# Optimization experiments

Measured on AMD Instinct MI355X. Metric: run time of the kernel, lower is better.

Reference implementation:

```python
import jax, jax.numpy as jnp
import numpy as np

B, T, HID = 1, 2048, 1024
H, D, S, KMAX = 16, 64, 64, 8


def local_attention(q, k, v, W):
    # lucidrains LocalAttention: causal, look_backward=1, autopad, scale=D**-0.5
    b, h, t, d = q.shape
    pad = (-t) % W
    qp = jnp.pad(q, ((0, 0), (0, 0), (0, pad), (0, 0)))
    kp = jnp.pad(k, ((0, 0), (0, 0), (0, pad), (0, 0)))
    vp = jnp.pad(v, ((0, 0), (0, 0), (0, pad), (0, 0)))
    tp = t + pad
    nw = tp // W
    qw = qp.reshape(b, h, nw, W, d)
    kw = kp.reshape(b, h, nw, W, d)
    vw = vp.reshape(b, h, nw, W, d)

    def look_back(x):  # prepend previous window (zeros for window 0)
        prev = jnp.pad(x, ((0, 0), (0, 0), (1, 0), (0, 0), (0, 0)))[:, :, :nw]
        return jnp.concatenate([prev, x], axis=3)  # (b,h,nw,2W,d)

    kk, vv = look_back(kw), look_back(vw)
    pos = jnp.arange(tp).reshape(nw, W)
    kpos = jnp.concatenate(
        [jnp.pad(pos, ((1, 0), (0, 0)), constant_values=-1)[:nw], pos], axis=1)  # (nw,2W)
    scores = jnp.einsum('bhnwd,bhnkd->bhnwk', qw, kk) * (d ** -0.5)
    valid = (pos[:, :, None] >= kpos[:, None, :]) & (kpos[:, None, :] >= 0)
    scores = jnp.where(valid[None, None], scores, -jnp.finfo(scores.dtype).max)
    probs = jax.nn.softmax(scores, axis=-1)
    out = jnp.einsum('bhnwk,bhnkd->bhnwd', probs, vv).reshape(b, h, tp, d)
    return out[:, :, :t]


def setup_inputs() -> dict:
    key = jax.random.key(0)
    ks = jax.random.split(key, 9)
    sd = 0.02
    return {
        'hidden_states': jax.random.normal(ks[0], (B, T, HID), jnp.float32),
        'Wq': jax.random.normal(ks[1], (HID, H * D), jnp.float32) * sd,
        'Wk': jax.random.normal(ks[2], (HID, H * D), jnp.float32) * sd,
        'Wv': jax.random.normal(ks[3], (HID, H * D), jnp.float32) * sd,
        'Wo': jax.random.normal(ks[4], (H * D, HID), jnp.float32) * sd,
        'Wc': jax.random.normal(ks[5], (S * D, D), jnp.float32) * sd,
        'bc': jax.random.normal(ks[6], (D,), jnp.float32) * sd,
        'k_scale': jnp.ones((1, H, 1), jnp.float32),
        'k_bias': jnp.zeros((1, H, 1), jnp.float32),
        'Wg': jax.random.normal(ks[7], (HID, 3 * H), jnp.float32) * sd,
        'bg': jax.random.normal(ks[8], (3 * H,), jnp.float32) * sd,
    }


def reference(hidden_states, Wq, Wk, Wv, Wo, Wc, bc, k_scale, k_bias, Wg, bg):
    b, t, _ = hidden_states.shape
    scale = D ** -0.5
    q = (hidden_states @ Wq).reshape(b, t, H, D).transpose(0, 2, 1, 3)
    k = (hidden_states @ Wk).reshape(b, t, H, D).transpose(0, 2, 1, 3)
    v = (hidden_states @ Wv).reshape(b, t, H, D).transpose(0, 2, 1, 3)

    sw_out = local_attention(q, k, v, S)

    pad = (-t) % S
    qp = jnp.pad(q, ((0, 0), (0, 0), (0, pad), (0, 0)))
    kp = jnp.pad(k, ((0, 0), (0, 0), (0, pad), (0, 0)))
    vp = jnp.pad(v, ((0, 0), (0, 0), (0, pad), (0, 0)))
    tp = t + pad
    nb = tp // S

    # compressed branch: shared compress MLP for k and v (same weights in torch)
    k_blk = kp.reshape(b, H, nb, S * D)
    v_blk = vp.reshape(b, H, nb, S * D)
    kc = jax.nn.gelu(k_blk @ Wc + bc, approximate=False)  # (b,H,nb,D)
    vc = jax.nn.gelu(v_blk @ Wc + bc, approximate=False)

    importance = jnp.einsum('bhid,bhjd->bhij', qp, kc) * scale  # (b,H,tp,nb)
    comp_probs = jax.nn.softmax(importance, axis=-1)
    comp_out = jnp.einsum('bhij,bhjd->bhid', comp_probs, vc)[:, :, :t]

    # block scores, entropy-driven dynamic top-k
    block_scores = importance.reshape(b, H, nb, S, nb).mean(axis=3)  # (b,H,nb,nb)
    block_probs = jax.nn.softmax(block_scores, axis=-1)
    entropy = -jnp.sum(block_probs * jnp.log(block_probs + 1e-9), axis=-1)
    max_entropy = jnp.log(jnp.float32(nb))
    norm_entropy = entropy / (max_entropy + 1e-9)  # (b,H,nb)
    k_logit = k_scale * norm_entropy + k_bias
    k_ratio = jax.nn.sigmoid(k_logit)
    dynamic_k = jnp.clip(KMAX * k_ratio, 1, KMAX).astype(jnp.int32)
    avg_k = dynamic_k.astype(jnp.float32).mean()

    _, topk_idx = jax.lax.top_k(block_scores, KMAX)  # (b,H,nb,KMAX)
    k_mask = jnp.arange(KMAX)[None, None, None, :] < dynamic_k[..., None]
    sel = (topk_idx[..., None] == jnp.arange(nb)) & k_mask[..., None]  # (b,H,nb,K,nb)
    mask = sel.any(axis=-2) | jnp.eye(nb, dtype=bool)  # (b,H,nb,nb)
    sparse_mask = jnp.repeat(jnp.repeat(mask, S, axis=2), S, axis=3)  # (b,H,tp,tp)

    attn = jnp.einsum('bhid,bhjd->bhij', qp, kp) * scale
    attn = jnp.where(sparse_mask, attn, -jnp.finfo(attn.dtype).max)
    fine_probs = jax.nn.softmax(attn, axis=-1)
    fine_out = jnp.einsum('bhij,bhjd->bhid', fine_probs, vp)[:, :, :t]

    gate = jax.nn.sigmoid(hidden_states @ Wg + bg)  # (b,t,3H)
    gate = gate.reshape(b, t, H, 3).transpose(0, 2, 1, 3)  # (b,H,t,3)
    combined = jnp.stack([sw_out, comp_out, fine_out], axis=-1)  # (b,H,t,D,3)
    out = jnp.einsum('bhnds,bhns->bhnd', combined, gate)
    merged = out.transpose(0, 2, 1, 3).reshape(b, t, H * D)
    output = merged @ Wo
    return output, avg_k, k_ratio, norm_entropy
```

## Files before the change

### kernel.cpp

```cpp
#include <hip/hip_runtime.h>
#include <math.h>

#define TT 2048
#define NH 16
#define HD 64
#define NB 32
#define HIDDEN 1024

typedef short s8v __attribute__((ext_vector_type(8)));
typedef float f4v __attribute__((ext_vector_type(4)));

__device__ __forceinline__ unsigned short f2bf(float x){
  unsigned u = __float_as_uint(x);
  unsigned r = (u + 0x7fffu + ((u>>16)&1u)) >> 16;
  return (unsigned short)r;
}
__device__ __forceinline__ float bf2f(unsigned short b){
  return __uint_as_float(((unsigned)b)<<16);
}
__device__ __forceinline__ void bsplit(float x, unsigned short& h, unsigned short& l){
  h = f2bf(x);
  l = f2bf(x - bf2f(h));
}

__device__ __forceinline__ float rmax32(float v){
#pragma unroll
  for(int o=16;o>0;o>>=1) v = fmaxf(v, __shfl_xor(v,o,32));
  return v;
}
__device__ __forceinline__ float rsum32(float v){
#pragma unroll
  for(int o=16;o>0;o>>=1) v += __shfl_xor(v,o,32);
  return v;
}

__global__ __launch_bounds__(256) void split_hs_k(
    const float* __restrict__ hs, unsigned short* __restrict__ hh, unsigned short* __restrict__ hl)
{
  int i = (blockIdx.x*256 + threadIdx.x)*4;
  float4 x = *(const float4*)(hs + i);
  ushort4 hv, lv;
  bsplit(x.x, hv.x, lv.x); bsplit(x.y, hv.y, lv.y);
  bsplit(x.z, hv.z, lv.z); bsplit(x.w, hv.w, lv.w);
  *(ushort4*)(hh + i) = hv;
  *(ushort4*)(hl + i) = lv;
}

__global__ __launch_bounds__(256) void prep_w_k(
    const float* __restrict__ Wq, const float* __restrict__ Wk,
    const float* __restrict__ Wv, const float* __restrict__ Wo,
    unsigned short* __restrict__ wth, unsigned short* __restrict__ wtl,
    unsigned short* __restrict__ woth)
{
  int z = blockIdx.z;
  const float* W = (z==0)?Wq:((z==1)?Wk:((z==2)?Wv:Wo));
  int k0 = blockIdx.y*64, n0 = blockIdx.x*64;
  __shared__ float L[64][68];
  int t = threadIdx.x;
  int rr = t>>2, cg = t&3;
  const float* src = W + (size_t)(k0+rr)*1024 + n0 + cg*16;
  float4 a = *(const float4*)(src);
  float4 b = *(const float4*)(src+4);
  float4 c = *(const float4*)(src+8);
  float4 d = *(const float4*)(src+12);
  *(float4*)&L[rr][cg*16+0]  = a;
  *(float4*)&L[rr][cg*16+4]  = b;
  *(float4*)&L[rr][cg*16+8]  = c;
  *(float4*)&L[rr][cg*16+12] = d;
  __syncthreads();
  int nr = t>>2, kg = t&3;
  unsigned short hb[16], lb[16];
#pragma unroll
  for(int j=0;j<16;j++){
    float v = L[kg*16+j][nr];
    bsplit(v, hb[j], lb[j]);
  }
  if(z<3){
    size_t orow = ((size_t)z*1024 + n0 + nr)*1024 + k0 + kg*16;
    *(ushort4*)(wth+orow+0)  = make_ushort4(hb[0],hb[1],hb[2],hb[3]);
    *(ushort4*)(wth+orow+4)  = make_ushort4(hb[4],hb[5],hb[6],hb[7]);
    *(ushort4*)(wth+orow+8)  = make_ushort4(hb[8],hb[9],hb[10],hb[11]);
    *(ushort4*)(wth+orow+12) = make_ushort4(hb[12],hb[13],hb[14],hb[15]);
    *(ushort4*)(wtl+orow+0)  = make_ushort4(lb[0],lb[1],lb[2],lb[3]);
    *(ushort4*)(wtl+orow+4)  = make_ushort4(lb[4],lb[5],lb[6],lb[7]);
    *(ushort4*)(wtl+orow+8)  = make_ushort4(lb[8],lb[9],lb[10],lb[11]);
    *(ushort4*)(wtl+orow+12) = make_ushort4(lb[12],lb[13],lb[14],lb[15]);
  }else{
    size_t orow = ((size_t)n0 + nr)*1024 + k0 + kg*16;
    *(ushort4*)(woth+orow+0)  = make_ushort4(hb[0],hb[1],hb[2],hb[3]);
    *(ushort4*)(woth+orow+4)  = make_ushort4(hb[4],hb[5],hb[6],hb[7]);
    *(ushort4*)(woth+orow+8)  = make_ushort4(hb[8],hb[9],hb[10],hb[11]);
    *(ushort4*)(woth+orow+12) = make_ushort4(hb[12],hb[13],hb[14],hb[15]);
  }
}

__global__ __launch_bounds__(256) void prep_wc_k(
    const float* __restrict__ Wc, unsigned short* __restrict__ wcth, unsigned short* __restrict__ wctl)
{
  int k0 = blockIdx.x*64;
  __shared__ float L[64][68];
  int t = threadIdx.x;
  int rr = t>>2, cg = t&3;
  const float* src = Wc + (size_t)(k0+rr)*64 + cg*16;
  float4 a = *(const float4*)(src);
  float4 b = *(const float4*)(src+4);
  float4 c = *(const float4*)(src+8);
  float4 d = *(const float4*)(src+12);
  *(float4*)&L[rr][cg*16+0]  = a;
  *(float4*)&L[rr][cg*16+4]  = b;
  *(float4*)&L[rr][cg*16+8]  = c;
  *(float4*)&L[rr][cg*16+12] = d;
  __syncthreads();
  int nr = t>>2, kg = t&3;
  unsigned short hb[16], lb[16];
#pragma unroll
  for(int j=0;j<16;j++){
    float v = L[kg*16+j][nr];
    bsplit(v, hb[j], lb[j]);
  }
  size_t orow = (size_t)nr*4096 + k0 + kg*16;
  *(ushort4*)(wcth+orow+0)  = make_ushort4(hb[0],hb[1],hb[2],hb[3]);
  *(ushort4*)(wcth+orow+4)  = make_ushort4(hb[4],hb[5],hb[6],hb[7]);
  *(ushort4*)(wcth+orow+8)  = make_ushort4(hb[8],hb[9],hb[10],hb[11]);
  *(ushort4*)(wcth+orow+12) = make_ushort4(hb[12],hb[13],hb[14],hb[15]);
  *(ushort4*)(wctl+orow+0)  = make_ushort4(lb[0],lb[1],lb[2],lb[3]);
  *(ushort4*)(wctl+orow+4)  = make_ushort4(lb[4],lb[5],lb[6],lb[7]);
  *(ushort4*)(wctl+orow+8)  = make_ushort4(lb[8],lb[9],lb[10],lb[11]);
  *(ushort4*)(wctl+orow+12) = make_ushort4(lb[12],lb[13],lb[14],lb[15]);
}

#define LROW 40
__global__ __launch_bounds__(256) void mfma_qkv_k(
    const unsigned short* __restrict__ ahg, const unsigned short* __restrict__ alg,
    const unsigned short* __restrict__ bhg, const unsigned short* __restrict__ blg,
    float* __restrict__ C0, float* __restrict__ C1, float* __restrict__ C2)
{
  __shared__ unsigned short Ah[128*LROW], Al[128*LROW], Bh[128*LROW], Bl[128*LROW];
  int tid = threadIdx.x;
  int bn = blockIdx.x*128, bm = blockIdx.y*128;
  bool tp = (blockIdx.x < 16);
  int sr = tid>>2, skg = tid&3;
  const unsigned short* gA  = ahg + (size_t)(bm+sr)*HIDDEN + skg*8;
  const unsigned short* gAl = alg + (size_t)(bm+sr)*HIDDEN + skg*8;
  const unsigned short* gB  = bhg + (size_t)(bn+sr)*HIDDEN + skg*8;
  const unsigned short* gBl = blg + (size_t)(bn+sr)*HIDDEN + skg*8;
  int wv = tid>>6, ln = tid&63;
  int wm = (wv&1)*64, wn = (wv>>1)*64;
  int fr = ln&15, fq = ln>>4;
  int wlds = sr*LROW + skg*8;
  f4v acc[4][4] = {};
  for(int k0=0;k0<HIDDEN;k0+=32){
    s8v a0 = *(const s8v*)(gA + k0);
    s8v a1 = *(const s8v*)(gA + 65536 + k0);
    s8v b0 = *(const s8v*)(gB + k0);
    s8v b1 = *(const s8v*)(gB + 65536 + k0);
    s8v a0l, a1l, b0l, b1l;
    if(tp){
      a0l = *(const s8v*)(gAl + k0);
      a1l = *(const s8v*)(gAl + 65536 + k0);
      b0l = *(const s8v*)(gBl + k0);
      b1l = *(const s8v*)(gBl + 65536 + k0);
    }
    __syncthreads();
    *(s8v*)&Ah[wlds] = a0; *(s8v*)&Ah[wlds + 64*LROW] = a1;
    *(s8v*)&Bh[wlds] = b0; *(s8v*)&Bh[wlds + 64*LROW] = b1;
    if(tp){
      *(s8v*)&Al[wlds] = a0l; *(s8v*)&Al[wlds + 64*LROW] = a1l;
      *(s8v*)&Bl[wlds] = b0l; *(s8v*)&Bl[wlds + 64*LROW] = b1l;
    }
    __syncthreads();
    s8v af[4], bf[4], tf;
#pragma unroll
    for(int i=0;i<4;i++) af[i] = *(const s8v*)&Ah[(wm+i*16+fr)*LROW + fq*8];
#pragma unroll
    for(int i=0;i<4;i++) bf[i] = *(const s8v*)&Bh[(wn+i*16+fr)*LROW + fq*8];
#pragma unroll
    for(int i=0;i<4;i++)
#pragma unroll
      for(int j=0;j<4;j++)
        acc[i][j] = __builtin_amdgcn_mfma_f32_16x16x32_bf16(af[i], bf[j], acc[i][j], 0,0,0);
    if(tp){
#pragma unroll
      for(int i=0;i<4;i++){
        tf = *(const s8v*)&Al[(wm+i*16+fr)*LROW + fq*8];
#pragma unroll
        for(int j=0;j<4;j++)
          acc[i][j] = __builtin_amdgcn_mfma_f32_16x16x32_bf16(tf, bf[j], acc[i][j], 0,0,0);
      }
#pragma unroll
      for(int j=0;j<4;j++){
        tf = *(const s8v*)&Bl[(wn+j*16+fr)*LROW + fq*8];
#pragma unroll
        for(int i=0;i<4;i++)
          acc[i][j] = __builtin_amdgcn_mfma_f32_16x16x32_bf16(af[i], tf, acc[i][j], 0,0,0);
      }
    }
  }
  int z = bn >> 10;
  float* C = (z==0)?C0:((z==1)?C1:C2);
#pragma unroll
  for(int i=0;i<4;i++){
    int mb = bm + wm + i*16 + fq*4;
#pragma unroll
    for(int j=0;j<4;j++){
      int n = bn + wn + j*16 + fr;
      int n1 = n & 1023, hd = n1>>6, d = n1&63;
      float* dst = C + ((size_t)hd*TT + mb)*HD + d;
#pragma unroll
      for(int r=0;r<4;r++) dst[(size_t)r*HD] = acc[i][j][r];
    }
  }
}

__global__ __launch_bounds__(256) void conv_qkv(
    const float* __restrict__ qb, const float* __restrict__ kb, const float* __restrict__ vb,
    unsigned short* __restrict__ qbh, unsigned short* __restrict__ qbl,
    unsigned short* __restrict__ kbh, unsigned short* __restrict__ kbl,
    unsigned short* __restrict__ vbh)
{
  int z = blockIdx.y;
  const float* s = (z==0)?qb:((z==1)?kb:vb);
  unsigned short* dh = (z==0)?qbh:((z==1)?kbh:vbh);
  unsigned short* dl = (z==0)?qbl:kbl;
  size_t i = ((size_t)blockIdx.x*256 + threadIdx.x)*8;
  float4 a = *(const float4*)(s+i);
  float4 b = *(const float4*)(s+i+4);
  float xs[8] = {a.x,a.y,a.z,a.w,b.x,b.y,b.z,b.w};
  s8v rh, rl;
#pragma unroll
  for(int u=0;u<8;u++){
    unsigned short h = f2bf(xs[u]);
    rh[u] = (short)h;
    rl[u] = (short)f2bf(xs[u] - bf2f(h));
  }
  *(s8v*)(dh+i) = rh;
  if(z<2) *(s8v*)(dl+i) = rl;
}

__global__ __launch_bounds__(256) void conv_vt(
    const float* __restrict__ vb, unsigned short* __restrict__ vth)
{
  int tt = blockIdx.x, h = blockIdx.y;
  __shared__ float L[64][68];
  int t = threadIdx.x;
  int row = t>>2, dg = (t&3)*16;
  const float* src = vb + ((size_t)h*TT + tt*64 + row)*HD + dg;
  float4 a = *(const float4*)(src);
  float4 b = *(const float4*)(src+4);
  float4 c = *(const float4*)(src+8);
  float4 e = *(const float4*)(src+12);
  *(float4*)&L[row][dg+0]  = a;
  *(float4*)&L[row][dg+4]  = b;
  *(float4*)&L[row][dg+8]  = c;
  *(float4*)&L[row][dg+12] = e;
  __syncthreads();
  int d = t>>2, kg = (t&3)*16;
  s8v r0, r1;
#pragma unroll
  for(int u=0;u<8;u++)  r0[u] = (short)f2bf(L[kg+u][d]);
#pragma unroll
  for(int u=0;u<8;u++)  r1[u] = (short)f2bf(L[kg+8+u][d]);
  unsigned short* dst = vth + ((size_t)h*HD + d)*TT + tt*64 + kg;
  *(s8v*)(dst)   = r0;
  *(s8v*)(dst+8) = r1;
}

#define CROW 40
__global__ __launch_bounds__(256) void mfma_compress_k(
    const unsigned short* __restrict__ kbh, const unsigned short* __restrict__ kbl,
    const unsigned short* __restrict__ vbh,
    const unsigned short* __restrict__ wcth, const unsigned short* __restrict__ wctl,
    float* __restrict__ ccpart)
{
  __shared__ unsigned short As[64*CROW], Al[64*CROW], Bs[64*CROW], Bl[64*CROW];
  int chunk = blockIdx.x;
  int mt = blockIdx.y;
  bool isK = (mt < 8);
  const unsigned short* Ag  = isK ? (kbh + (size_t)mt*262144) : (vbh + (size_t)(mt-8)*262144);
  const unsigned short* Agl = kbl + (size_t)(isK ? mt : 0)*262144;
  int tid = threadIdx.x;
  int sr = tid>>2, skg = (tid&3)*8;
  int k0b = chunk*512;
  const unsigned short* gA  = Ag  + (size_t)sr*4096 + k0b + skg;
  const unsigned short* gAl = Agl + (size_t)sr*4096 + k0b + skg;
  const unsigned short* gB  = wcth + (size_t)sr*4096 + k0b + skg;
  const unsigned short* gBl = wctl + (size_t)sr*4096 + k0b + skg;
  int wv = tid>>6, ln = tid&63;
  int fr = ln&15, fq = ln>>4;
  int wlds = sr*CROW + skg;
  f4v acc[4] = {};
  for(int ks=0; ks<512; ks+=32){
    s8v a0 = *(const s8v*)(gA + ks);
    s8v b0 = *(const s8v*)(gB + ks);
    s8v b1 = *(const s8v*)(gBl + ks);
    s8v a1 = {};
    if(isK) a1 = *(const s8v*)(gAl + ks);
    __syncthreads();
    *(s8v*)&As[wlds] = a0;
    *(s8v*)&Bs[wlds] = b0;
    *(s8v*)&Bl[wlds] = b1;
    if(isK) *(s8v*)&Al[wlds] = a1;
    __syncthreads();
    s8v bfh = *(const s8v*)&Bs[(wv*16+fr)*CROW + fq*8];
    s8v bfl = *(const s8v*)&Bl[(wv*16+fr)*CROW + fq*8];
#pragma unroll
    for(int m=0;m<4;m++){
      s8v af = *(const s8v*)&As[(m*16+fr)*CROW + fq*8];
      acc[m] = __builtin_amdgcn_mfma_f32_16x16x32_bf16(af, bfh, acc[m], 0,0,0);
      acc[m] = __builtin_amdgcn_mfma_f32_16x16x32_bf16(af, bfl, acc[m], 0,0,0);
      if(isK){
        s8v afl = *(const s8v*)&Al[(m*16+fr)*CROW + fq*8];
        acc[m] = __builtin_amdgcn_mfma_f32_16x16x32_bf16(afl, bfh, acc[m], 0,0,0);
      }
    }
  }
  float* dst = ccpart + ((size_t)chunk*1024 + mt*64)*64;
#pragma unroll
  for(int m=0;m<4;m++)
#pragma unroll
    for(int r=0;r<4;r++)
      dst[(size_t)(m*16+fq*4+r)*64 + wv*16 + fr] = acc[m][r];
}

__global__ __launch_bounds__(256) void compress_fin(
    const float* __restrict__ ccpart, const float* __restrict__ bcp,
    unsigned short* __restrict__ kch, unsigned short* __restrict__ kcl,
    unsigned short* __restrict__ vcth)
{
  int idx = blockIdx.x*256 + threadIdx.x;
  int row = idx>>6, col = idx&63;
  float s = 0.f;
#pragma unroll
  for(int c=0;c<8;c++) s += ccpart[(size_t)c*65536 + idx];
  s += bcp[col];
  float g = 0.5f*s*(1.f+erff(s*0.70710678118654752f));
  if(row < 512){
    unsigned short hi = f2bf(g);
    kch[idx] = hi;
    kcl[idx] = f2bf(g - bf2f(hi));
  }else{
    int r = row - 512;
    int h = r>>5, j = r&31;
    vcth[((size_t)h*64 + col)*32 + j] = f2bf(g);
  }
}

__global__ __launch_bounds__(256) void comp_attn_mfma(
    const unsigned short* __restrict__ qbh, const unsigned short* __restrict__ qbl,
    const unsigned short* __restrict__ kch, const unsigned short* __restrict__ kcl,
    const unsigned short* __restrict__ vcth,
    float* __restrict__ imp, float* __restrict__ comp)
{
  __shared__ unsigned short Pl[4*16*40];
  int tid = threadIdx.x;
  int wave = __builtin_amdgcn_readfirstlane(tid>>6);
  int ln = tid&63;
  int fr = ln&15, fq = ln>>4;
  int i = blockIdx.x, h = blockIdx.y;

  const unsigned short* qrh = qbh + ((size_t)h*TT + i*64 + wave*16 + fr)*HD + fq*8;
  const unsigned short* qrl = qbl + ((size_t)h*TT + i*64 + wave*16 + fr)*HD + fq*8;
  s8v bh0 = *(const s8v*)(qrh);
  s8v bh1 = *(const s8v*)(qrh + 32);
  s8v bl0 = *(const s8v*)(qrl);
  s8v bl1 = *(const s8v*)(qrl + 32);

  f4v sv[2] = {};
#pragma unroll
  for(int mt=0;mt<2;mt++){
    const unsigned short* ar = kch + ((size_t)h*32 + mt*16 + fr)*HD + fq*8;
    const unsigned short* al = kcl + ((size_t)h*32 + mt*16 + fr)*HD + fq*8;
    s8v ah0 = *(const s8v*)(ar);
    s8v ah1 = *(const s8v*)(ar + 32);
    s8v al0 = *(const s8v*)(al);
    s8v al1 = *(const s8v*)(al + 32);
    sv[mt] = __builtin_amdgcn_mfma_f32_16x16x32_bf16(ah0, bh0, sv[mt], 0,0,0);
    sv[mt] = __builtin_amdgcn_mfma_f32_16x16x32_bf16(ah1, bh1, sv[mt], 0,0,0);
    sv[mt] = __builtin_amdgcn_mfma_f32_16x16x32_bf16(al0, bh0, sv[mt], 0,0,0);
    sv[mt] = __builtin_amdgcn_mfma_f32_16x16x32_bf16(al1, bh1, sv[mt], 0,0,0);
    sv[mt] = __builtin_amdgcn_mfma_f32_16x16x32_bf16(ah0, bl0, sv[mt], 0,0,0);
    sv[mt] = __builtin_amdgcn_mfma_f32_16x16x32_bf16(ah1, bl1, sv[mt], 0,0,0);
  }
  int t = i*64 + wave*16 + fr;
  float* impr = imp + ((size_t)h*TT + t)*NB;
  float mx = -3.4e38f;
#pragma unroll
  for(int mt=0;mt<2;mt++)
#pragma unroll
    for(int r=0;r<4;r++){
      float s = sv[mt][r]*0.125f;
      sv[mt][r] = s;
      impr[mt*16 + fq*4 + r] = s;
      mx = fmaxf(mx, s);
    }
  mx = fmaxf(mx, __shfl_xor(mx,16,64));
  mx = fmaxf(mx, __shfl_xor(mx,32,64));
  unsigned short* Pw = Pl + wave*16*40;
  float es = 0.f;
#pragma unroll
  for(int mt=0;mt<2;mt++)
#pragma unroll
    for(int r=0;r<4;r++){
      float p = __expf(sv[mt][r] - mx);
      es += p;
      Pw[fr*40 + mt*16 + fq*4 + r] = f2bf(p);
    }
  es += __shfl_xor(es,16,64);
  es += __shfl_xor(es,32,64);

  s8v ap = *(const s8v*)&Pw[fr*40 + fq*8];
  f4v acc[4] = {};
#pragma unroll
  for(int nt=0;nt<4;nt++){
    s8v bv = *(const s8v*)(vcth + ((size_t)h*64 + nt*16 + fr)*32 + fq*8);
    acc[nt] = __builtin_amdgcn_mfma_f32_16x16x32_bf16(ap, bv, acc[nt], 0,0,0);
  }
  float lv[4];
#pragma unroll
  for(int r=0;r<4;r++) lv[r] = __shfl(es, fq*4+r, 64);
#pragma unroll
  for(int nt=0;nt<4;nt++)
#pragma unroll
    for(int r=0;r<4;r++){
      int tq = i*64 + wave*16 + fq*4 + r;
      comp[((size_t)h*TT + tq)*HD + nt*16 + fr] = acc[nt][r]/lv[r];
    }
}

__global__ __launch_bounds__(256) void mfma_proj_k(
    const unsigned short* __restrict__ ahg, const unsigned short* __restrict__ bhg,
    float* __restrict__ C)
{
  __shared__ unsigned short Ah[128*LROW], Bh[128*LROW];
  int tid = threadIdx.x;
  int bn = blockIdx.x*128, bm = blockIdx.y*128;
  int sr = tid>>2, skg = tid&3;
  const unsigned short* gA = ahg + (size_t)(bm+sr)*HIDDEN + skg*8;
  const unsigned short* gB = bhg + (size_t)(bn+sr)*HIDDEN + skg*8;
  int wv = tid>>6, ln = tid&63;
  int wm = (wv&1)*64, wn = (wv>>1)*64;
  int fr = ln&15, fq = ln>>4;
  int wlds = sr*LROW + skg*8;
  f4v acc[4][4] = {};
  for(int k0=0;k0<HIDDEN;k0+=32){
    s8v a0 = *(const s8v*)(gA + k0);
    s8v a1 = *(const s8v*)(gA + 65536 + k0);
    s8v b0 = *(const s8v*)(gB + k0);
    s8v b1 = *(const s8v*)(gB + 65536 + k0);
    __syncthreads();
    *(s8v*)&Ah[wlds] = a0; *(s8v*)&Ah[wlds + 64*LROW] = a1;
    *(s8v*)&Bh[wlds] = b0; *(s8v*)&Bh[wlds + 64*LROW] = b1;
    __syncthreads();
    s8v af[4], bf[4];
#pragma unroll
    for(int i=0;i<4;i++) af[i] = *(const s8v*)&Ah[(wm+i*16+fr)*LROW + fq*8];
#pragma unroll
    for(int i=0;i<4;i++) bf[i] = *(const s8v*)&Bh[(wn+i*16+fr)*LROW + fq*8];
#pragma unroll
    for(int i=0;i<4;i++)
#pragma unroll
      for(int j=0;j<4;j++)
        acc[i][j] = __builtin_amdgcn_mfma_f32_16x16x32_bf16(af[i], bf[j], acc[i][j], 0,0,0);
  }
#pragma unroll
  for(int i=0;i<4;i++){
    int mb = bm + wm + i*16 + fq*4;
#pragma unroll
    for(int j=0;j<4;j++){
      int n = bn + wn + j*16 + fr;
      float* dst = C + (size_t)mb*HIDDEN + n;
#pragma unroll
      for(int r=0;r<4;r++) dst[(size_t)r*HIDDEN] = acc[i][j][r];
    }
  }
}

__global__ __launch_bounds__(256) void gate_kernel(
    const float* __restrict__ hs, const float* __restrict__ Wg, const float* __restrict__ bg,
    float* __restrict__ gatep)
{
  int t = blockIdx.x;
  __shared__ float row[1024];
  __shared__ float red[4][64];
  int tid = threadIdx.x;
  *(float4*)(row + tid*4) = *(const float4*)(hs + (size_t)t*HIDDEN + tid*4);
  __syncthreads();
  int n = tid & 63, part = tid>>6;
  float s = 0.f;
  if(n < 48){
    const float* w = Wg + n;
    for(int kx = part*256; kx < part*256+256; kx++)
      s += row[kx]*w[(size_t)kx*48];
  }
  red[part][n] = s;
  __syncthreads();
  if(part==0 && n<48){
    float x = red[0][n]+red[1][n]+red[2][n]+red[3][n] + bg[n];
    gatep[(size_t)t*48 + n] = 1.f/(1.f+expf(-x));
  }
}

__global__ __launch_bounds__(256) void block_stats(
    const float* __restrict__ imp, const float* __restrict__ ksc, const float* __restrict__ kbi,
    unsigned* __restrict__ maskb, float* __restrict__ dkf,
    float* __restrict__ out_kratio, float* __restrict__ out_nent)
{
  int hb = blockIdx.x; int h = hb>>5, i = hb&31;
  int tid = threadIdx.x; int j = tid&31, p = tid>>5;
  const float* base = imp + ((size_t)h*TT + i*64)*NB;
  float s = 0.f;
  for(int t2=p*8; t2<p*8+8; t2++) s += base[(size_t)t2*NB + j];
  __shared__ float red[8][32];
  red[p][j] = s;
  __syncthreads();
  if(tid < 32){
    float bs = 0.f;
#pragma unroll
    for(int pp=0; pp<8; pp++) bs += red[pp][j];
    bs *= (1.f/64.f);
    float m = rmax32(bs);
    float e = expf(bs - m);
    float se = rsum32(e);
    float prob = e/se;
    float ent = rsum32(-prob * logf(prob + 1e-9f));
    float nent = ent / (3.4657359027997265f + 1e-9f);
    float kl = ksc[h]*nent + kbi[h];
    float kr = 1.f/(1.f + expf(-kl));
    float dkfl = fminf(fmaxf(8.f*kr, 1.f), 8.f);
    int dk = (int)dkfl;
    unsigned sel = 0u;
    for(int r=0;r<dk;r++){
      bool unpicked = ((sel>>j)&1u)==0u;
      float cand = unpicked ? bs : -3.4e38f;
      float mx = rmax32(cand);
      unsigned long long b = __ballot(cand == mx);
      int idxsel = __ffsll(b & 0xffffffffull) - 1;
      sel |= (1u<<idxsel);
    }
    sel |= (1u<<i);
    if(j==0){
      maskb[hb] = sel;
      dkf[hb] = (float)dk;
      out_kratio[hb] = kr;
      out_nent[hb] = nent;
    }
  }
}

__global__ __launch_bounds__(256) void avgk_kernel(const float* __restrict__ dkf, float* __restrict__ outp){
  __shared__ float red[256];
  int tid=threadIdx.x;
  red[tid] = dkf[tid] + dkf[tid+256];
  __syncthreads();
  for(int s=128;s>0;s>>=1){ if(tid<s) red[tid]+=red[tid+s]; __syncthreads(); }
  if(tid==0) outp[0] = red[0] * (1.f/512.f);
}

__global__ __launch_bounds__(256) void attn_mfma(
    const unsigned short* __restrict__ qbh, const unsigned short* __restrict__ kbh,
    const unsigned short* __restrict__ vth,
    const unsigned* __restrict__ maskb, float* __restrict__ outp, int causal_local)
{
  __shared__ unsigned short Kb[64*72];
  __shared__ unsigned short Vt[64*72];
  __shared__ unsigned short Pl[4*16*72];
  int tid = threadIdx.x;
  int wave = __builtin_amdgcn_readfirstlane(tid>>6);
  int ln = tid & 63;
  int fr = ln & 15, fq = ln >> 4;
  int hb = blockIdx.x; int h = hb>>5, i = hb&31;
  unsigned mb = causal_local ? ((1u<<i) | (i ? (1u<<(i-1)) : 0u)) : maskb[hb];

  const unsigned short* qrow = qbh + ((size_t)h*TT + i*64 + wave*16 + fr)*HD + fq*8;
  s8v bq0 = *(const s8v*)(qrow);
  s8v bq1 = *(const s8v*)(qrow + 32);

  f4v acc_o[4] = {};
  float m_run = -3.4e38f;
  float l_run = 0.f;

  int srow = tid>>2, sg = (tid&3)*16;
  unsigned short* Pw = Pl + wave*16*72;

  for(int j=0;j<NB;j++){
    if(!((mb>>j)&1u)) continue;
    __syncthreads();
    {
      const unsigned short* ks_ = kbh + ((size_t)h*TT + j*64 + srow)*HD + sg;
      *(s8v*)&Kb[srow*72 + sg]     = *(const s8v*)(ks_);
      *(s8v*)&Kb[srow*72 + sg + 8] = *(const s8v*)(ks_ + 8);
      const unsigned short* vs_ = vth + ((size_t)h*HD + srow)*TT + j*64 + sg;
      *(s8v*)&Vt[srow*72 + sg]     = *(const s8v*)(vs_);
      *(s8v*)&Vt[srow*72 + sg + 8] = *(const s8v*)(vs_ + 8);
    }
    __syncthreads();

    f4v sv[4] = {};
#pragma unroll
    for(int mt=0;mt<4;mt++){
      s8v ak0 = *(const s8v*)&Kb[(mt*16+fr)*72 + fq*8];
      s8v ak1 = *(const s8v*)&Kb[(mt*16+fr)*72 + fq*8 + 32];
      sv[mt] = __builtin_amdgcn_mfma_f32_16x16x32_bf16(ak0, bq0, sv[mt], 0,0,0);
      sv[mt] = __builtin_amdgcn_mfma_f32_16x16x32_bf16(ak1, bq1, sv[mt], 0,0,0);
    }
    bool diag = (causal_local!=0) && (j==i);
    int qpos = wave*16 + fr;
#pragma unroll
    for(int mt=0;mt<4;mt++){
#pragma unroll
      for(int r=0;r<4;r++){
        float s = sv[mt][r]*0.125f;
        if(diag && (mt*16 + fq*4 + r) > qpos) s = -3.4e38f;
        sv[mt][r] = s;
      }
    }
    float mx = -3.4e38f;
#pragma unroll
    for(int mt=0;mt<4;mt++)
#pragma unroll
      for(int r=0;r<4;r++) mx = fmaxf(mx, sv[mt][r]);
    mx = fmaxf(mx, __shfl_xor(mx,16,64));
    mx = fmaxf(mx, __shfl_xor(mx,32,64));
    float mnew = fmaxf(m_run, mx);
    float es = 0.f;
#pragma unroll
    for(int mt=0;mt<4;mt++)
#pragma unroll
      for(int r=0;r<4;r++){
        float p = __expf(sv[mt][r] - mnew);
        es += p;
        Pw[fr*72 + mt*16 + fq*4 + r] = f2bf(p);
      }
    es += __shfl_xor(es,16,64);
    es += __shfl_xor(es,32,64);
    float alpha = __expf(m_run - mnew);
    l_run = l_run*alpha + es;
    m_run = mnew;
    float av[4];
#pragma unroll
    for(int r=0;r<4;r++) av[r] = __shfl(alpha, fq*4+r, 64);
#pragma unroll
    for(int nt=0;nt<4;nt++)
#pragma unroll
      for(int r=0;r<4;r++) acc_o[nt][r] *= av[r];
    __syncthreads();

    s8v ap0 = *(const s8v*)&Pw[fr*72 + fq*8];
    s8v ap1 = *(const s8v*)&Pw[fr*72 + fq*8 + 32];
#pragma unroll
    for(int nt=0;nt<4;nt++){
      s8v bv0 = *(const s8v*)&Vt[(nt*16+fr)*72 + fq*8];
      s8v bv1 = *(const s8v*)&Vt[(nt*16+fr)*72 + fq*8 + 32];
      acc_o[nt] = __builtin_amdgcn_mfma_f32_16x16x32_bf16(ap0, bv0, acc_o[nt], 0,0,0);
      acc_o[nt] = __builtin_amdgcn_mfma_f32_16x16x32_bf16(ap1, bv1, acc_o[nt], 0,0,0);
    }
  }
  float lv[4];
#pragma unroll
  for(int r=0;r<4;r++) lv[r] = __shfl(l_run, fq*4+r, 64);
#pragma unroll
  for(int nt=0;nt<4;nt++){
#pragma unroll
    for(int r=0;r<4;r++){
      int t = i*64 + wave*16 + fq*4 + r;
      int d = nt*16 + fr;
      outp[((size_t)h*TT + t)*HD + d] = acc_o[nt][r] / lv[r];
    }
  }
}

__global__ __launch_bounds__(256) void combine_kernel(
    const float* __restrict__ swo, const float* __restrict__ comp, const float* __restrict__ fino,
    const float* __restrict__ gatep, unsigned short* __restrict__ mergedh)
{
  int idx = blockIdx.x*256 + threadIdx.x;
  int t = idx>>10, c = idx & 1023;
  int h = c>>6, d = c&63;
  const float* g = gatep + (size_t)t*48 + h*3;
  size_t a = ((size_t)h*TT + t)*HD + d;
  mergedh[idx] = f2bf(g[0]*swo[a] + g[1]*comp[a] + g[2]*fino[a]);
}

extern "C" void kernel_launch(void* const* d_in, const int* in_sizes, int n_in,
                              void* d_out, int out_size, void* d_ws, size_t ws_size,
                              hipStream_t stream) {
  (void)in_sizes; (void)n_in; (void)out_size; (void)ws_size;
  const float* hs  = (const float*)d_in[0];
  const float* Wq  = (const float*)d_in[1];
  const float* Wk  = (const float*)d_in[2];
  const float* Wv  = (const float*)d_in[3];
  const float* Wo  = (const float*)d_in[4];
  const float* Wc  = (const float*)d_in[5];
  const float* bcp = (const float*)d_in[6];
  const float* ksc = (const float*)d_in[7];
  const float* kbi = (const float*)d_in[8];
  const float* Wg  = (const float*)d_in[9];
  const float* bg  = (const float*)d_in[10];
  float* out = (float*)d_out;

  float* ws = (float*)d_ws;
  float* qb     = ws;
  float* kb     = qb + 2097152;
  float* vb     = kb + 2097152;
  float* gatep  = vb + 2097152;
  unsigned short* kch  = (unsigned short*)(gatep + 98304);
  unsigned short* kcl  = kch + 32768;
  unsigned short* vcth = kcl + 32768;
  float* imp    = gatep + 98304 + 65536;
  float* comp   = imp + 1048576;
  float* swo    = comp + 2097152;
  float* fino   = swo + 2097152;
  unsigned short* mergedh = (unsigned short*)(fino + 2097152);
  float* dkf    = fino + 2097152 + 1048576;
  unsigned* maskb = (unsigned*)(dkf + 512);
  unsigned short* woth = (unsigned short*)(dkf + 1024);
  unsigned short* qbh = (unsigned short*)(dkf + 1024 + 524288);
  unsigned short* kbh = qbh + 2097152;
  unsigned short* vth = kbh + 2097152;
  unsigned short* qbl = vth + 2097152;
  unsigned short* kbl = qbl + 2097152;
  unsigned short* vbh = kbl + 2097152;
  unsigned short* wcth = vbh + 2097152;
  unsigned short* wctl = wcth + 262144;
  float* ccpart = (float*)(wctl + 262144);

  unsigned short* hsh = (unsigned short*)comp;
  unsigned short* hsl = (unsigned short*)(comp + 1048576);
  unsigned short* wth = (unsigned short*)swo;
  unsigned short* wtl = (unsigned short*)(swo + 1572864);

  float* out_avgk   = out + 2097152;
  float* out_kratio = out + 2097153;
  float* out_nent   = out + 2097665;

  split_hs_k<<<dim3(2048), 256, 0, stream>>>(hs, hsh, hsl);
  prep_w_k<<<dim3(16,16,4), 256, 0, stream>>>(Wq, Wk, Wv, Wo, wth, wtl, woth);
  prep_wc_k<<<dim3(64), 256, 0, stream>>>(Wc, wcth, wctl);
  mfma_qkv_k<<<dim3(24,16), 256, 0, stream>>>(hsh, hsl, wth, wtl, qb, kb, vb);
  conv_qkv<<<dim3(1024,3), 256, 0, stream>>>(qb, kb, vb, qbh, qbl, kbh, kbl, vbh);
  conv_vt<<<dim3(32,16), 256, 0, stream>>>(vb, vth);
  gate_kernel<<<dim3(2048), 256, 0, stream>>>(hs, Wg, bg, gatep);
  mfma_compress_k<<<dim3(8,16), 256, 0, stream>>>(kbh, kbl, vbh, wcth, wctl, ccpart);
  compress_fin<<<dim3(256), 256, 0, stream>>>(ccpart, bcp, kch, kcl, vcth);
  comp_attn_mfma<<<dim3(32,16), 256, 0, stream>>>(qbh, qbl, kch, kcl, vcth, imp, comp);
  block_stats<<<dim3(512), 256, 0, stream>>>(imp, ksc, kbi, maskb, dkf, out_kratio, out_nent);
  avgk_kernel<<<dim3(1), 256, 0, stream>>>(dkf, out_avgk);
  attn_mfma<<<dim3(512), 256, 0, stream>>>(qbh, kbh, vth, maskb, swo, 1);
  attn_mfma<<<dim3(512), 256, 0, stream>>>(qbh, kbh, vth, maskb, fino, 0);
  combine_kernel<<<dim3(8192), 256, 0, stream>>>(swo, comp, fino, gatep, mergedh);
  mfma_proj_k<<<dim3(8,16), 256, 0, stream>>>(mergedh, woth, out);
}
```

Baseline: 259.3 us.

## Fuse prep kernels, QKV conversion epilogue, and sliding/fine attention with gating combine

Merges the three weight/activation prep kernels into one launch. The QKV GEMM epilogue now writes the bf16 hi/lo splits directly, which removes the fp32 QKV buffers and the conv_qkv pass, and conv_vt now reads bf16. The sliding-window and selected-block attention passes become one kernel that loads each K/V tile once for both softmax streams and applies the gate combine inline, so the swo/fino intermediates and combine_kernel are gone. The cost is more registers and LDS in the fused attention kernel, and uncoalesced 2-byte scattered stores in the GEMM epilogue.

```diff
diff --git a/kernel.cpp b/kernel.cpp
--- a/kernel.cpp
+++ b/kernel.cpp
@@ -34,106 +34,110 @@
   return v;
 }
 
-__global__ __launch_bounds__(256) void split_hs_k(
-    const float* __restrict__ hs, unsigned short* __restrict__ hh, unsigned short* __restrict__ hl)
-{
-  int i = (blockIdx.x*256 + threadIdx.x)*4;
-  float4 x = *(const float4*)(hs + i);
-  ushort4 hv, lv;
-  bsplit(x.x, hv.x, lv.x); bsplit(x.y, hv.y, lv.y);
-  bsplit(x.z, hv.z, lv.z); bsplit(x.w, hv.w, lv.w);
-  *(ushort4*)(hh + i) = hv;
-  *(ushort4*)(hl + i) = lv;
-}
-
-__global__ __launch_bounds__(256) void prep_w_k(
+__global__ __launch_bounds__(256) void prep_all(
+    const float* __restrict__ hs,
     const float* __restrict__ Wq, const float* __restrict__ Wk,
     const float* __restrict__ Wv, const float* __restrict__ Wo,
+    const float* __restrict__ Wc,
+    unsigned short* __restrict__ hh, unsigned short* __restrict__ hl,
     unsigned short* __restrict__ wth, unsigned short* __restrict__ wtl,
-    unsigned short* __restrict__ woth)
-{
-  int z = blockIdx.z;
-  const float* W = (z==0)?Wq:((z==1)?Wk:((z==2)?Wv:Wo));
-  int k0 = blockIdx.y*64, n0 = blockIdx.x*64;
+    unsigned short* __restrict__ woth,
+    unsigned short* __restrict__ wcth, unsigned short* __restrict__ wctl)
+{
   __shared__ float L[64][68];
+  int bx = blockIdx.x;
   int t = threadIdx.x;
-  int rr = t>>2, cg = t&3;
-  const float* src = W + (size_t)(k0+rr)*1024 + n0 + cg*16;
-  float4 a = *(const float4*)(src);
-  float4 b = *(const float4*)(src+4);
-  float4 c = *(const float4*)(src+8);
-  float4 d = *(const float4*)(src+12);
-  *(float4*)&L[rr][cg*16+0]  = a;
-  *(float4*)&L[rr][cg*16+4]  = b;
-  *(float4*)&L[rr][cg*16+8]  = c;
-  *(float4*)&L[rr][cg*16+12] = d;
-  __syncthreads();
-  int nr = t>>2, kg = t&3;
-  unsigned short hb[16], lb[16];
-#pragma unroll
-  for(int j=0;j<16;j++){
-    float v = L[kg*16+j][nr];
-    bsplit(v, hb[j], lb[j]);
-  }
-  if(z<3){
-    size_t orow = ((size_t)z*1024 + n0 + nr)*1024 + k0 + kg*16;
-    *(ushort4*)(wth+orow+0)  = make_ushort4(hb[0],hb[1],hb[2],hb[3]);
-    *(ushort4*)(wth+orow+4)  = make_ushort4(hb[4],hb[5],hb[6],hb[7]);
-    *(ushort4*)(wth+orow+8)  = make_ushort4(hb[8],hb[9],hb[10],hb[11]);
-    *(ushort4*)(wth+orow+12) = make_ushort4(hb[12],hb[13],hb[14],hb[15]);
-    *(ushort4*)(wtl+orow+0)  = make_ushort4(lb[0],lb[1],lb[2],lb[3]);
-    *(ushort4*)(wtl+orow+4)  = make_ushort4(lb[4],lb[5],lb[6],lb[7]);
-    *(ushort4*)(wtl+orow+8)  = make_ushort4(lb[8],lb[9],lb[10],lb[11]);
-    *(ushort4*)(wtl+orow+12) = make_ushort4(lb[12],lb[13],lb[14],lb[15]);
-  }else{
-    size_t orow = ((size_t)n0 + nr)*1024 + k0 + kg*16;
-    *(ushort4*)(woth+orow+0)  = make_ushort4(hb[0],hb[1],hb[2],hb[3]);
-    *(ushort4*)(woth+orow+4)  = make_ushort4(hb[4],hb[5],hb[6],hb[7]);
-    *(ushort4*)(woth+orow+8)  = make_ushort4(hb[8],hb[9],hb[10],hb[11]);
-    *(ushort4*)(woth+orow+12) = make_ushort4(hb[12],hb[13],hb[14],hb[15]);
-  }
-}
-
-__global__ __launch_bounds__(256) void prep_wc_k(
-    const float* __restrict__ Wc, unsigned short* __restrict__ wcth, unsigned short* __restrict__ wctl)
-{
-  int k0 = blockIdx.x*64;
-  __shared__ float L[64][68];
-  int t = threadIdx.x;
-  int rr = t>>2, cg = t&3;
-  const float* src = Wc + (size_t)(k0+rr)*64 + cg*16;
-  float4 a = *(const float4*)(src);
-  float4 b = *(const float4*)(src+4);
-  float4 c = *(const float4*)(src+8);
-  float4 d = *(const float4*)(src+12);
-  *(float4*)&L[rr][cg*16+0]  = a;
-  *(float4*)&L[rr][cg*16+4]  = b;
-  *(float4*)&L[rr][cg*16+8]  = c;
-  *(float4*)&L[rr][cg*16+12] = d;
-  __syncthreads();
-  int nr = t>>2, kg = t&3;
-  unsigned short hb[16], lb[16];
-#pragma unroll
-  for(int j=0;j<16;j++){
-    float v = L[kg*16+j][nr];
-    bsplit(v, hb[j], lb[j]);
-  }
-  size_t orow = (size_t)nr*4096 + k0 + kg*16;
-  *(ushort4*)(wcth+orow+0)  = make_ushort4(hb[0],hb[1],hb[2],hb[3]);
-  *(ushort4*)(wcth+orow+4)  = make_ushort4(hb[4],hb[5],hb[6],hb[7]);
-  *(ushort4*)(wcth+orow+8)  = make_ushort4(hb[8],hb[9],hb[10],hb[11]);
-  *(ushort4*)(wcth+orow+12) = make_ushort4(hb[12],hb[13],hb[14],hb[15]);
-  *(ushort4*)(wctl+orow+0)  = make_ushort4(lb[0],lb[1],lb[2],lb[3]);
-  *(ushort4*)(wctl+orow+4)  = make_ushort4(lb[4],lb[5],lb[6],lb[7]);
-  *(ushort4*)(wctl+orow+8)  = make_ushort4(lb[8],lb[9],lb[10],lb[11]);
-  *(ushort4*)(wctl+orow+12) = make_ushort4(lb[12],lb[13],lb[14],lb[15]);
+  if(bx < 2048){
+    int i = (bx*256 + t)*4;
+    float4 x = *(const float4*)(hs + i);
+    ushort4 hv, lv;
+    bsplit(x.x, hv.x, lv.x); bsplit(x.y, hv.y, lv.y);
+    bsplit(x.z, hv.z, lv.z); bsplit(x.w, hv.w, lv.w);
+    *(ushort4*)(hh + i) = hv;
+    *(ushort4*)(hl + i) = lv;
+    return;
+  }
+  if(bx < 3072){
+    int idx = bx - 2048;
+    int z = idx>>8, ky = (idx>>4)&15, nx = idx&15;
+    const float* W = (z==0)?Wq:((z==1)?Wk:((z==2)?Wv:Wo));
+    int k0 = ky*64, n0 = nx*64;
+    int rr = t>>2, cg = t&3;
+    const float* src = W + (size_t)(k0+rr)*1024 + n0 + cg*16;
+    float4 a = *(const float4*)(src);
+    float4 b = *(const float4*)(src+4);
+    float4 c = *(const float4*)(src+8);
+    float4 d = *(const float4*)(src+12);
+    *(float4*)&L[rr][cg*16+0]  = a;
+    *(float4*)&L[rr][cg*16+4]  = b;
+    *(float4*)&L[rr][cg*16+8]  = c;
+    *(float4*)&L[rr][cg*16+12] = d;
+    __syncthreads();
+    int nr = t>>2, kg = t&3;
+    unsigned short hb[16], lb[16];
+#pragma unroll
+    for(int j=0;j<16;j++){
+      float v = L[kg*16+j][nr];
+      bsplit(v, hb[j], lb[j]);
+    }
+    if(z<3){
+      size_t orow = ((size_t)z*1024 + n0 + nr)*1024 + k0 + kg*16;
+      *(ushort4*)(wth+orow+0)  = make_ushort4(hb[0],hb[1],hb[2],hb[3]);
+      *(ushort4*)(wth+orow+4)  = make_ushort4(hb[4],hb[5],hb[6],hb[7]);
+      *(ushort4*)(wth+orow+8)  = make_ushort4(hb[8],hb[9],hb[10],hb[11]);
+      *(ushort4*)(wth+orow+12) = make_ushort4(hb[12],hb[13],hb[14],hb[15]);
+      *(ushort4*)(wtl+orow+0)  = make_ushort4(lb[0],lb[1],lb[2],lb[3]);
+      *(ushort4*)(wtl+orow+4)  = make_ushort4(lb[4],lb[5],lb[6],lb[7]);
+      *(ushort4*)(wtl+orow+8)  = make_ushort4(lb[8],lb[9],lb[10],lb[11]);
+      *(ushort4*)(wtl+orow+12) = make_ushort4(lb[12],lb[13],lb[14],lb[15]);
+    }else{
+      size_t orow = ((size_t)n0 + nr)*1024 + k0 + kg*16;
+      *(ushort4*)(woth+orow+0)  = make_ushort4(hb[0],hb[1],hb[2],hb[3]);
+      *(ushort4*)(woth+orow+4)  = make_ushort4(hb[4],hb[5],hb[6],hb[7]);
+      *(ushort4*)(woth+orow+8)  = make_ushort4(hb[8],hb[9],hb[10],hb[11]);
+      *(ushort4*)(woth+orow+12) = make_ushort4(hb[12],hb[13],hb[14],hb[15]);
+    }
+    return;
+  }
+  {
+    int k0 = (bx - 3072)*64;
+    int rr = t>>2, cg = t&3;
+    const float* src = Wc + (size_t)(k0+rr)*64 + cg*16;
+    float4 a = *(const float4*)(src);
+    float4 b = *(const float4*)(src+4);
+    float4 c = *(const float4*)(src+8);
+    float4 d = *(const float4*)(src+12);
+    *(float4*)&L[rr][cg*16+0]  = a;
+    *(float4*)&L[rr][cg*16+4]  = b;
+    *(float4*)&L[rr][cg*16+8]  = c;
+    *(float4*)&L[rr][cg*16+12] = d;
+    __syncthreads();
+    int nr = t>>2, kg = t&3;
+    unsigned short hb[16], lb[16];
+#pragma unroll
+    for(int j=0;j<16;j++){
+      float v = L[kg*16+j][nr];
+      bsplit(v, hb[j], lb[j]);
+    }
+    size_t orow = (size_t)nr*4096 + k0 + kg*16;
+    *(ushort4*)(wcth+orow+0)  = make_ushort4(hb[0],hb[1],hb[2],hb[3]);
+    *(ushort4*)(wcth+orow+4)  = make_ushort4(hb[4],hb[5],hb[6],hb[7]);
+    *(ushort4*)(wcth+orow+8)  = make_ushort4(hb[8],hb[9],hb[10],hb[11]);
+    *(ushort4*)(wcth+orow+12) = make_ushort4(hb[12],hb[13],hb[14],hb[15]);
+    *(ushort4*)(wctl+orow+0)  = make_ushort4(lb[0],lb[1],lb[2],lb[3]);
+    *(ushort4*)(wctl+orow+4)  = make_ushort4(lb[4],lb[5],lb[6],lb[7]);
+    *(ushort4*)(wctl+orow+8)  = make_ushort4(lb[8],lb[9],lb[10],lb[11]);
+    *(ushort4*)(wctl+orow+12) = make_ushort4(lb[12],lb[13],lb[14],lb[15]);
+  }
 }
 
 #define LROW 40
 __global__ __launch_bounds__(256) void mfma_qkv_k(
     const unsigned short* __restrict__ ahg, const unsigned short* __restrict__ alg,
     const unsigned short* __restrict__ bhg, const unsigned short* __restrict__ blg,
-    float* __restrict__ C0, float* __restrict__ C1, float* __restrict__ C2)
+    unsigned short* __restrict__ qbh, unsigned short* __restrict__ qbl,
+    unsigned short* __restrict__ kbh, unsigned short* __restrict__ kbl,
+    unsigned short* __restrict__ vbh)
 {
   __shared__ unsigned short Ah[128*LROW], Al[128*LROW], Bh[128*LROW], Bl[128*LROW];
   int tid = threadIdx.x;
@@ -197,7 +201,6 @@
     }
   }
   int z = bn >> 10;
-  float* C = (z==0)?C0:((z==1)?C1:C2);
 #pragma unroll
   for(int i=0;i<4;i++){
     int mb = bm + wm + i*16 + fq*4;
@@ -205,64 +208,70 @@
     for(int j=0;j<4;j++){
       int n = bn + wn + j*16 + fr;
       int n1 = n & 1023, hd = n1>>6, d = n1&63;
-      float* dst = C + ((size_t)hd*TT + mb)*HD + d;
-#pragma unroll
-      for(int r=0;r<4;r++) dst[(size_t)r*HD] = acc[i][j][r];
-    }
-  }
-}
-
-__global__ __launch_bounds__(256) void conv_qkv(
-    const float* __restrict__ qb, const float* __restrict__ kb, const float* __restrict__ vb,
-    unsigned short* __restrict__ qbh, unsigned short* __restrict__ qbl,
-    unsigned short* __restrict__ kbh, unsigned short* __restrict__ kbl,
-    unsigned short* __restrict__ vbh)
-{
-  int z = blockIdx.y;
-  const float* s = (z==0)?qb:((z==1)?kb:vb);
-  unsigned short* dh = (z==0)?qbh:((z==1)?kbh:vbh);
-  unsigned short* dl = (z==0)?qbl:kbl;
-  size_t i = ((size_t)blockIdx.x*256 + threadIdx.x)*8;
-  float4 a = *(const float4*)(s+i);
-  float4 b = *(const float4*)(s+i+4);
-  float xs[8] = {a.x,a.y,a.z,a.w,b.x,b.y,b.z,b.w};
-  s8v rh, rl;
-#pragma unroll
-  for(int u=0;u<8;u++){
-    unsigned short h = f2bf(xs[u]);
-    rh[u] = (short)h;
-    rl[u] = (short)f2bf(xs[u] - bf2f(h));
-  }
-  *(s8v*)(dh+i) = rh;
-  if(z<2) *(s8v*)(dl+i) = rl;
+      size_t base = ((size_t)hd*TT + mb)*HD + d;
+#pragma unroll
+      for(int r=0;r<4;r++){
+        float v = acc[i][j][r];
+        size_t a = base + (size_t)r*HD;
+        if(z==0){
+          unsigned short hi = f2bf(v);
+          qbh[a] = hi; qbl[a] = f2bf(v - bf2f(hi));
+        }else if(z==1){
+          unsigned short hi = f2bf(v);
+          kbh[a] = hi; kbl[a] = f2bf(v - bf2f(hi));
+        }else{
+          vbh[a] = f2bf(v);
+        }
+      }
+    }
+  }
 }
 
 __global__ __launch_bounds__(256) void conv_vt(
-    const float* __restrict__ vb, unsigned short* __restrict__ vth)
+    const unsigned short* __restrict__ vbh, unsigned short* __restrict__ vth)
 {
   int tt = blockIdx.x, h = blockIdx.y;
-  __shared__ float L[64][68];
+  __shared__ unsigned short L[64][72];
   int t = threadIdx.x;
   int row = t>>2, dg = (t&3)*16;
-  const float* src = vb + ((size_t)h*TT + tt*64 + row)*HD + dg;
-  float4 a = *(const float4*)(src);
-  float4 b = *(const float4*)(src+4);
-  float4 c = *(const float4*)(src+8);
-  float4 e = *(const float4*)(src+12);
-  *(float4*)&L[row][dg+0]  = a;
-  *(float4*)&L[row][dg+4]  = b;
-  *(float4*)&L[row][dg+8]  = c;
-  *(float4*)&L[row][dg+12] = e;
+  const unsigned short* src = vbh + ((size_t)h*TT + tt*64 + row)*HD + dg;
+  *(s8v*)&L[row][dg]   = *(const s8v*)(src);
+  *(s8v*)&L[row][dg+8] = *(const s8v*)(src+8);
   __syncthreads();
   int d = t>>2, kg = (t&3)*16;
   s8v r0, r1;
 #pragma unroll
-  for(int u=0;u<8;u++)  r0[u] = (short)f2bf(L[kg+u][d]);
-#pragma unroll
-  for(int u=0;u<8;u++)  r1[u] = (short)f2bf(L[kg+8+u][d]);
+  for(int u=0;u<8;u++)  r0[u] = (short)L[kg+u][d];
+#pragma unroll
+  for(int u=0;u<8;u++)  r1[u] = (short)L[kg+8+u][d];
   unsigned short* dst = vth + ((size_t)h*HD + d)*TT + tt*64 + kg;
   *(s8v*)(dst)   = r0;
   *(s8v*)(dst+8) = r1;
+}
+
+__global__ __launch_bounds__(256) void gate_kernel(
+    const float* __restrict__ hs, const float* __restrict__ Wg, const float* __restrict__ bg,
+    float* __restrict__ gatep)
+{
+  int t = blockIdx.x;
+  __shared__ float row[1024];
+  __shared__ float red[4][64];
+  int tid = threadIdx.x;
+  *(float4*)(row + tid*4) = *(const float4*)(hs + (size_t)t*HIDDEN + tid*4);
+  __syncthreads();
+  int n = tid & 63, part = tid>>6;
+  float s = 0.f;
+  if(n < 48){
+    const float* w = Wg + n;
+    for(int kx = part*256; kx < part*256+256; kx++)
+      s += row[kx]*w[(size_t)kx*48];
+  }
+  red[part][n] = s;
+  __syncthreads();
+  if(part==0 && n<48){
+    float x = red[0][n]+red[1][n]+red[2][n]+red[3][n] + bg[n];
+    gatep[(size_t)t*48 + n] = 1.f/(1.f+expf(-x));
+  }
 }
 
 #define CROW 40
@@ -427,79 +436,6 @@
     }
 }
 
-__global__ __launch_bounds__(256) void mfma_proj_k(
-    const unsigned short* __restrict__ ahg, const unsigned short* __restrict__ bhg,
-    float* __restrict__ C)
-{
-  __shared__ unsigned short Ah[128*LROW], Bh[128*LROW];
-  int tid = threadIdx.x;
-  int bn = blockIdx.x*128, bm = blockIdx.y*128;
-  int sr = tid>>2, skg = tid&3;
-  const unsigned short* gA = ahg + (size_t)(bm+sr)*HIDDEN + skg*8;
-  const unsigned short* gB = bhg + (size_t)(bn+sr)*HIDDEN + skg*8;
-  int wv = tid>>6, ln = tid&63;
-  int wm = (wv&1)*64, wn = (wv>>1)*64;
-  int fr = ln&15, fq = ln>>4;
-  int wlds = sr*LROW + skg*8;
-  f4v acc[4][4] = {};
-  for(int k0=0;k0<HIDDEN;k0+=32){
-    s8v a0 = *(const s8v*)(gA + k0);
-    s8v a1 = *(const s8v*)(gA + 65536 + k0);
-    s8v b0 = *(const s8v*)(gB + k0);
-    s8v b1 = *(const s8v*)(gB + 65536 + k0);
-    __syncthreads();
-    *(s8v*)&Ah[wlds] = a0; *(s8v*)&Ah[wlds + 64*LROW] = a1;
-    *(s8v*)&Bh[wlds] = b0; *(s8v*)&Bh[wlds + 64*LROW] = b1;
-    __syncthreads();
-    s8v af[4], bf[4];
-#pragma unroll
-    for(int i=0;i<4;i++) af[i] = *(const s8v*)&Ah[(wm+i*16+fr)*LROW + fq*8];
-#pragma unroll
-    for(int i=0;i<4;i++) bf[i] = *(const s8v*)&Bh[(wn+i*16+fr)*LROW + fq*8];
-#pragma unroll
-    for(int i=0;i<4;i++)
-#pragma unroll
-      for(int j=0;j<4;j++)
-        acc[i][j] = __builtin_amdgcn_mfma_f32_16x16x32_bf16(af[i], bf[j], acc[i][j], 0,0,0);
-  }
-#pragma unroll
-  for(int i=0;i<4;i++){
-    int mb = bm + wm + i*16 + fq*4;
-#pragma unroll
-    for(int j=0;j<4;j++){
-      int n = bn + wn + j*16 + fr;
-      float* dst = C + (size_t)mb*HIDDEN + n;
-#pragma unroll
-      for(int r=0;r<4;r++) dst[(size_t)r*HIDDEN] = acc[i][j][r];
-    }
-  }
-}
-
-__global__ __launch_bounds__(256) void gate_kernel(
-    const float* __restrict__ hs, const float* __restrict__ Wg, const float* __restrict__ bg,
-    float* __restrict__ gatep)
-{
-  int t = blockIdx.x;
-  __shared__ float row[1024];
-  __shared__ float red[4][64];
-  int tid = threadIdx.x;
-  *(float4*)(row + tid*4) = *(const float4*)(hs + (size_t)t*HIDDEN + tid*4);
-  __syncthreads();
-  int n = tid & 63, part = tid>>6;
-  float s = 0.f;
-  if(n < 48){
-    const float* w = Wg + n;
-    for(int kx = part*256; kx < part*256+256; kx++)
-      s += row[kx]*w[(size_t)kx*48];
-  }
-  red[part][n] = s;
-  __syncthreads();
-  if(part==0 && n<48){
-    float x = red[0][n]+red[1][n]+red[2][n]+red[3][n] + bg[n];
-    gatep[(size_t)t*48 + n] = 1.f/(1.f+expf(-x));
-  }
-}
-
 __global__ __launch_bounds__(256) void block_stats(
     const float* __restrict__ imp, const float* __restrict__ ksc, const float* __restrict__ kbi,
     unsigned* __restrict__ maskb, float* __restrict__ dkf,
@@ -556,31 +492,36 @@
   if(tid==0) outp[0] = red[0] * (1.f/512.f);
 }
 
-__global__ __launch_bounds__(256) void attn_mfma(
+__global__ __launch_bounds__(256) void attn_fused(
     const unsigned short* __restrict__ qbh, const unsigned short* __restrict__ kbh,
-    const unsigned short* __restrict__ vth,
-    const unsigned* __restrict__ maskb, float* __restrict__ outp, int causal_local)
+    const unsigned short* __restrict__ vth, const unsigned* __restrict__ maskb,
+    const float* __restrict__ comp, const float* __restrict__ gatep,
+    unsigned short* __restrict__ mergedh)
 {
   __shared__ unsigned short Kb[64*72];
   __shared__ unsigned short Vt[64*72];
-  __shared__ unsigned short Pl[4*16*72];
+  __shared__ unsigned short Pf[4*16*72];
+  __shared__ unsigned short Ps[4*16*72];
   int tid = threadIdx.x;
   int wave = __builtin_amdgcn_readfirstlane(tid>>6);
   int ln = tid & 63;
   int fr = ln & 15, fq = ln >> 4;
   int hb = blockIdx.x; int h = hb>>5, i = hb&31;
-  unsigned mb = causal_local ? ((1u<<i) | (i ? (1u<<(i-1)) : 0u)) : maskb[hb];
+  unsigned mb_s = (1u<<i) | (i ? (1u<<(i-1)) : 0u);
+  unsigned mb_f = maskb[hb];
+  unsigned mb = mb_s | mb_f;
 
   const unsigned short* qrow = qbh + ((size_t)h*TT + i*64 + wave*16 + fr)*HD + fq*8;
   s8v bq0 = *(const s8v*)(qrow);
   s8v bq1 = *(const s8v*)(qrow + 32);
 
-  f4v acc_o[4] = {};
-  float m_run = -3.4e38f;
-  float l_run = 0.f;
+  f4v acc_f[4] = {}, acc_s[4] = {};
+  float mf = -3.4e38f, lf = 0.f, ms = -3.4e38f, ls = 0.f;
 
   int srow = tid>>2, sg = (tid&3)*16;
-  unsigned short* Pw = Pl + wave*16*72;
+  unsigned short* Pfw = Pf + wave*16*72;
+  unsigned short* Psw = Ps + wave*16*72;
+  int qpos = wave*16 + fr;
 
   for(int j=0;j<NB;j++){
     if(!((mb>>j)&1u)) continue;
@@ -603,82 +544,177 @@
       sv[mt] = __builtin_amdgcn_mfma_f32_16x16x32_bf16(ak0, bq0, sv[mt], 0,0,0);
       sv[mt] = __builtin_amdgcn_mfma_f32_16x16x32_bf16(ak1, bq1, sv[mt], 0,0,0);
     }
-    bool diag = (causal_local!=0) && (j==i);
-    int qpos = wave*16 + fr;
-#pragma unroll
-    for(int mt=0;mt<4;mt++){
-#pragma unroll
-      for(int r=0;r<4;r++){
-        float s = sv[mt][r]*0.125f;
-        if(diag && (mt*16 + fq*4 + r) > qpos) s = -3.4e38f;
-        sv[mt][r] = s;
+#pragma unroll
+    for(int mt=0;mt<4;mt++)
+#pragma unroll
+      for(int r=0;r<4;r++) sv[mt][r] *= 0.125f;
+
+    bool in_f = ((mb_f>>j)&1u) != 0u;
+    bool in_s = (j==i) || (j+1==i);
+
+    if(in_f){
+      float mx = -3.4e38f;
+#pragma unroll
+      for(int mt=0;mt<4;mt++)
+#pragma unroll
+        for(int r=0;r<4;r++) mx = fmaxf(mx, sv[mt][r]);
+      mx = fmaxf(mx, __shfl_xor(mx,16,64));
+      mx = fmaxf(mx, __shfl_xor(mx,32,64));
+      float mnew = fmaxf(mf, mx);
+      float es = 0.f;
+#pragma unroll
+      for(int mt=0;mt<4;mt++)
+#pragma unroll
+        for(int r=0;r<4;r++){
+          float p = __expf(sv[mt][r] - mnew);
+          es += p;
+          Pfw[fr*72 + mt*16 + fq*4 + r] = f2bf(p);
+        }
+      es += __shfl_xor(es,16,64);
+      es += __shfl_xor(es,32,64);
+      float alpha = __expf(mf - mnew);
+      lf = lf*alpha + es;
+      mf = mnew;
+      float av[4];
+#pragma unroll
+      for(int r=0;r<4;r++) av[r] = __shfl(alpha, fq*4+r, 64);
+#pragma unroll
+      for(int nt=0;nt<4;nt++)
+#pragma unroll
+        for(int r=0;r<4;r++) acc_f[nt][r] *= av[r];
+    }
+    if(in_s){
+      if(j==i){
+#pragma unroll
+        for(int mt=0;mt<4;mt++)
+#pragma unroll
+          for(int r=0;r<4;r++)
+            if((mt*16 + fq*4 + r) > qpos) sv[mt][r] = -3.4e38f;
       }
-    }
-    float mx = -3.4e38f;
-#pragma unroll
-    for(int mt=0;mt<4;mt++)
-#pragma unroll
-      for(int r=0;r<4;r++) mx = fmaxf(mx, sv[mt][r]);
-    mx = fmaxf(mx, __shfl_xor(mx,16,64));
-    mx = fmaxf(mx, __shfl_xor(mx,32,64));
-    float mnew = fmaxf(m_run, mx);
-    float es = 0.f;
-#pragma unroll
-    for(int mt=0;mt<4;mt++)
-#pragma unroll
-      for(int r=0;r<4;r++){
-        float p = __expf(sv[mt][r] - mnew);
-        es += p;
-        Pw[fr*72 + mt*16 + fq*4 + r] = f2bf(p);
+      float mx = -3.4e38f;
+#pragma unroll
+      for(int mt=0;mt<4;mt++)
+#pragma unroll
+        for(int r=0;r<4;r++) mx = fmaxf(mx, sv[mt][r]);
+      mx = fmaxf(mx, __shfl_xor(mx,16,64));
+      mx = fmaxf(mx, __shfl_xor(mx,32,64));
+      float mnew = fmaxf(ms, mx);
+      float es = 0.f;
+#pragma unroll
+      for(int mt=0;mt<4;mt++)
+#pragma unroll
+        for(int r=0;r<4;r++){
+          float p = __expf(sv[mt][r] - mnew);
+          es += p;
+          Psw[fr*72 + mt*16 + fq*4 + r] = f2bf(p);
+        }
+      es += __shfl_xor(es,16,64);
+      es += __shfl_xor(es,32,64);
+      float alpha = __expf(ms - mnew);
+      ls = ls*alpha + es;
+      ms = mnew;
+      float av[4];
+#pragma unroll
+      for(int r=0;r<4;r++) av[r] = __shfl(alpha, fq*4+r, 64);
+#pragma unroll
+      for(int nt=0;nt<4;nt++)
+#pragma unroll
+        for(int r=0;r<4;r++) acc_s[nt][r] *= av[r];
+    }
+
+    if(in_f){
+      s8v ap0 = *(const s8v*)&Pfw[fr*72 + fq*8];
+      s8v ap1 = *(const s8v*)&Pfw[fr*72 + fq*8 + 32];
+#pragma unroll
+      for(int nt=0;nt<4;nt++){
+        s8v bv0 = *(const s8v*)&Vt[(nt*16+fr)*72 + fq*8];
+        s8v bv1 = *(const s8v*)&Vt[(nt*16+fr)*72 + fq*8 + 32];
+        acc_f[nt] = __builtin_amdgcn_mfma_f32_16x16x32_bf16(ap0, bv0, acc_f[nt], 0,0,0);
+        acc_f[nt] = __builtin_amdgcn_mfma_f32_16x16x32_bf16(ap1, bv1, acc_f[nt], 0,0,0);
       }
-    es += __shfl_xor(es,16,64);
-    es += __shfl_xor(es,32,64);
-    float alpha = __expf(m_run - mnew);
-    l_run = l_run*alpha + es;
-    m_run = mnew;
-    float av[4];
-#pragma unroll
-    for(int r=0;r<4;r++) av[r] = __shfl(alpha, fq*4+r, 64);
-#pragma unroll
-    for(int nt=0;nt<4;nt++)
-#pragma unroll
-      for(int r=0;r<4;r++) acc_o[nt][r] *= av[r];
-    __syncthreads();
-
-    s8v ap0 = *(const s8v*)&Pw[fr*72 + fq*8];
-    s8v ap1 = *(const s8v*)&Pw[fr*72 + fq*8 + 32];
-#pragma unroll
-    for(int nt=0;nt<4;nt++){
-      s8v bv0 = *(const s8v*)&Vt[(nt*16+fr)*72 + fq*8];
-      s8v bv1 = *(const s8v*)&Vt[(nt*16+fr)*72 + fq*8 + 32];
-      acc_o[nt] = __builtin_amdgcn_mfma_f32_16x16x32_bf16(ap0, bv0, acc_o[nt], 0,0,0);
-      acc_o[nt] = __builtin_amdgcn_mfma_f32_16x16x32_bf16(ap1, bv1, acc_o[nt], 0,0,0);
-    }
-  }
-  float lv[4];
-#pragma unroll
-  for(int r=0;r<4;r++) lv[r] = __shfl(l_run, fq*4+r, 64);
+    }
+    if(in_s){
+      s8v ap0 = *(const s8v*)&Psw[fr*72 + fq*8];
+      s8v ap1 = *(const s8v*)&Psw[fr*72 + fq*8 + 32];
+#pragma unroll
+      for(int nt=0;nt<4;nt++){
+        s8v bv0 = *(const s8v*)&Vt[(nt*16+fr)*72 + fq*8];
+        s8v bv1 = *(const s8v*)&Vt[(nt*16+fr)*72 + fq*8 + 32];
+        acc_s[nt] = __builtin_amdgcn_mfma_f32_16x16x32_bf16(ap0, bv0, acc_s[nt], 0,0,0);
+        acc_s[nt] = __builtin_amdgcn_mfma_f32_16x16x32_bf16(ap1, bv1, acc_s[nt], 0,0,0);
+      }
+    }
+  }
+
+  float lvf[4], lvs[4], g0[4], g1[4], g2[4];
+#pragma unroll
+  for(int r=0;r<4;r++){
+    lvf[r] = __shfl(lf, fq*4+r, 64);
+    lvs[r] = __shfl(ls, fq*4+r, 64);
+    int t = i*64 + wave*16 + fq*4 + r;
+    const float* g = gatep + (size_t)t*48 + h*3;
+    g0[r] = g[0]; g1[r] = g[1]; g2[r] = g[2];
+  }
 #pragma unroll
   for(int nt=0;nt<4;nt++){
 #pragma unroll
     for(int r=0;r<4;r++){
       int t = i*64 + wave*16 + fq*4 + r;
       int d = nt*16 + fr;
-      outp[((size_t)h*TT + t)*HD + d] = acc_o[nt][r] / lv[r];
-    }
-  }
-}
-
-__global__ __launch_bounds__(256) void combine_kernel(
-    const float* __restrict__ swo, const float* __restrict__ comp, const float* __restrict__ fino,
-    const float* __restrict__ gatep, unsigned short* __restrict__ mergedh)
-{
-  int idx = blockIdx.x*256 + threadIdx.x;
-  int t = idx>>10, c = idx & 1023;
-  int h = c>>6, d = c&63;
-  const float* g = gatep + (size_t)t*48 + h*3;
-  size_t a = ((size_t)h*TT + t)*HD + d;
-  mergedh[idx] = f2bf(g[0]*swo[a] + g[1]*comp[a] + g[2]*fino[a]);
+      float of = acc_f[nt][r] / lvf[r];
+      float os = acc_s[nt][r] / lvs[r];
+      float cp = comp[((size_t)h*TT + t)*HD + d];
+      mergedh[(size_t)t*1024 + h*64 + d] = f2bf(g0[r]*os + g1[r]*cp + g2[r]*of);
+    }
+  }
+}
+
+__global__ __launch_bounds__(256) void mfma_proj_k(
+    const unsigned short* __restrict__ ahg, const unsigned short* __restrict__ bhg,
+    float* __restrict__ C)
+{
+  __shared__ unsigned short Ah[128*LROW], Bh[128*LROW];
+  int tid = threadIdx.x;
+  int bn = blockIdx.x*128, bm = blockIdx.y*128;
+  int sr = tid>>2, skg = tid&3;
+  const unsigned short* gA = ahg + (size_t)(bm+sr)*HIDDEN + skg*8;
+  const unsigned short* gB = bhg + (size_t)(bn+sr)*HIDDEN + skg*8;
+  int wv = tid>>6, ln = tid&63;
+  int wm = (wv&1)*64, wn = (wv>>1)*64;
+  int fr = ln&15, fq = ln>>4;
+  int wlds = sr*LROW + skg*8;
+  f4v acc[4][4] = {};
+  for(int k0=0;k0<HIDDEN;k0+=32){
+    s8v a0 = *(const s8v*)(gA + k0);
+    s8v a1 = *(const s8v*)(gA + 65536 + k0);
+    s8v b0 = *(const s8v*)(gB + k0);
+    s8v b1 = *(const s8v*)(gB + 65536 + k0);
+    __syncthreads();
+    *(s8v*)&Ah[wlds] = a0; *(s8v*)&Ah[wlds + 64*LROW] = a1;
+    *(s8v*)&Bh[wlds] = b0; *(s8v*)&Bh[wlds + 64*LROW] = b1;
+    __syncthreads();
+    s8v af[4], bf[4];
+#pragma unroll
+    for(int i=0;i<4;i++) af[i] = *(const s8v*)&Ah[(wm+i*16+fr)*LROW + fq*8];
+#pragma unroll
+    for(int i=0;i<4;i++) bf[i] = *(const s8v*)&Bh[(wn+i*16+fr)*LROW + fq*8];
+#pragma unroll
+    for(int i=0;i<4;i++)
+#pragma unroll
+      for(int j=0;j<4;j++)
+        acc[i][j] = __builtin_amdgcn_mfma_f32_16x16x32_bf16(af[i], bf[j], acc[i][j], 0,0,0);
+  }
+#pragma unroll
+  for(int i=0;i<4;i++){
+    int mb = bm + wm + i*16 + fq*4;
+#pragma unroll
+    for(int j=0;j<4;j++){
+      int n = bn + wn + j*16 + fr;
+      float* dst = C + (size_t)mb*HIDDEN + n;
+#pragma unroll
+      for(int r=0;r<4;r++) dst[(size_t)r*HIDDEN] = acc[i][j][r];
+    }
+  }
 }
 
 extern "C" void kernel_launch(void* const* d_in, const int* in_sizes, int n_in,
@@ -699,54 +735,48 @@
   float* out = (float*)d_out;
 
   float* ws = (float*)d_ws;
-  float* qb     = ws;
-  float* kb     = qb + 2097152;
-  float* vb     = kb + 2097152;
-  float* gatep  = vb + 2097152;
+  float* gatep  = ws;
   unsigned short* kch  = (unsigned short*)(gatep + 98304);
   unsigned short* kcl  = kch + 32768;
   unsigned short* vcth = kcl + 32768;
   float* imp    = gatep + 98304 + 65536;
   float* comp   = imp + 1048576;
-  float* swo    = comp + 2097152;
-  float* fino   = swo + 2097152;
-  unsigned short* mergedh = (unsigned short*)(fino + 2097152);
-  float* dkf    = fino + 2097152 + 1048576;
+  float* wthf   = comp + 2097152;
+  float* wtlf   = wthf + 1572864;
+  unsigned short* mergedh = (unsigned short*)(wtlf + 1572864);
+  float* dkf    = wtlf + 1572864 + 1048576;
   unsigned* maskb = (unsigned*)(dkf + 512);
   unsigned short* woth = (unsigned short*)(dkf + 1024);
-  unsigned short* qbh = (unsigned short*)(dkf + 1024 + 524288);
-  unsigned short* kbh = qbh + 2097152;
-  unsigned short* vth = kbh + 2097152;
-  unsigned short* qbl = vth + 2097152;
-  unsigned short* kbl = qbl + 2097152;
-  unsigned short* vbh = kbl + 2097152;
-  unsigned short* wcth = vbh + 2097152;
+  unsigned short* qbh  = (unsigned short*)(dkf + 1024 + 524288);
+  unsigned short* qbl  = qbh + 2097152;
+  unsigned short* kbh  = qbl + 2097152;
+  unsigned short* kbl  = kbh + 2097152;
+  unsigned short* vbh  = kbl + 2097152;
+  unsigned short* vth  = vbh + 2097152;
+  unsigned short* wcth = vth + 2097152;
   unsigned short* wctl = wcth + 262144;
   float* ccpart = (float*)(wctl + 262144);
 
   unsigned short* hsh = (unsigned short*)comp;
   unsigned short* hsl = (unsigned short*)(comp + 1048576);
-  unsigned short* wth = (unsigned short*)swo;
-  unsigned short* wtl = (unsigned short*)(swo + 1572864);
+  unsigned short* wth = (unsigned short*)wthf;
+  unsigned short* wtl = (unsigned short*)wtlf;
 
   float* out_avgk   = out + 2097152;
   float* out_kratio = out + 2097153;
   float* out_nent   = out + 2097665;
 
-  split_hs_k<<<dim3(2048), 256, 0, stream>>>(hs, hsh, hsl);
-  prep_w_k<<<dim3(16,16,4), 256, 0, stream>>>(Wq, Wk, Wv, Wo, wth, wtl, woth);
-  prep_wc_k<<<dim3(64), 256, 0, stream>>>(Wc, wcth, wctl);
-  mfma_qkv_k<<<dim3(24,16), 256, 0, stream>>>(hsh, hsl, wth, wtl, qb, kb, vb);
-  conv_qkv<<<dim3(1024,3), 256, 0, stream>>>(qb, kb, vb, qbh, qbl, kbh, kbl, vbh);
-  conv_vt<<<dim3(32,16), 256, 0, stream>>>(vb, vth);
+  prep_all<<<dim3(3136), 256, 0, stream>>>(hs, Wq, Wk, Wv, Wo, Wc,
+                                           hsh, hsl, wth, wtl, woth, wcth, wctl);
+  mfma_qkv_k<<<dim3(24,16), 256, 0, stream>>>(hsh, hsl, wth, wtl,
+                                              qbh, qbl, kbh, kbl, vbh);
+  conv_vt<<<dim3(32,16), 256, 0, stream>>>(vbh, vth);
   gate_kernel<<<dim3(2048), 256, 0, stream>>>(hs, Wg, bg, gatep);
   mfma_compress_k<<<dim3(8,16), 256, 0, stream>>>(kbh, kbl, vbh, wcth, wctl, ccpart);
   compress_fin<<<dim3(256), 256, 0, stream>>>(ccpart, bcp, kch, kcl, vcth);
   comp_attn_mfma<<<dim3(32,16), 256, 0, stream>>>(qbh, qbl, kch, kcl, vcth, imp, comp);
   block_stats<<<dim3(512), 256, 0, stream>>>(imp, ksc, kbi, maskb, dkf, out_kratio, out_nent);
   avgk_kernel<<<dim3(1), 256, 0, stream>>>(dkf, out_avgk);
-  attn_mfma<<<dim3(512), 256, 0, stream>>>(qbh, kbh, vth, maskb, swo, 1);
-  attn_mfma<<<dim3(512), 256, 0, stream>>>(qbh, kbh, vth, maskb, fino, 0);
-  combine_kernel<<<dim3(8192), 256, 0, stream>>>(swo, comp, fino, gatep, mergedh);
+  attn_fused<<<dim3(512), 256, 0, stream>>>(qbh, kbh, vth, maskb, comp, gatep, mergedh);
   mfma_proj_k<<<dim3(8,16), 256, 0, stream>>>(mergedh, woth, out);
 }
```

Result: faster. 236.5 us (-8.8%).
